# Kernel tuning notes

Measured on AMD Instinct MI355X. Metric: run time of the kernel, lower is better.

## Reference

```python
import jax, jax.numpy as jnp
import numpy as np


def setup_inputs() -> dict:
    key = jax.random.key(0)
    k1, k2, k3, k4 = jax.random.split(key, 4)
    B, Cin, H, W = 16, 64, 96, 96
    D, O, KH, KW, S = 100, 256, 3, 3, 3
    x = jax.random.normal(k1, (B, Cin, H, W), dtype=jnp.float32)
    dictionary = jax.random.normal(k2, (D, Cin, KH, KW), dtype=jnp.float32) * 0.05
    lookup_coefficients = jax.random.normal(k3, (O, KH, KW, S), dtype=jnp.float32) * 0.1
    lookup_indices = jax.random.randint(k4, (O, KH, KW, S), 0, D, dtype=jnp.int64)
    return {
        "x": x,
        "dictionary": dictionary,
        "lookup_coefficients": lookup_coefficients,
        "lookup_indices": lookup_indices,
    }


def reference(x, dictionary, lookup_coefficients, lookup_indices):
    # Dense conv with the small dictionary: [B, Cin, H, W] x [D, Cin, kh, kw] -> [B, D, Oh, Ow]
    conv_out = jax.lax.conv_general_dilated(
        x, dictionary,
        window_strides=(1, 1),
        padding=((1, 1), (1, 1)),
        dimension_numbers=("NCHW", "OIHW", "NCHW"),
    )
    O = lookup_coefficients.shape[0]
    D = dictionary.shape[0]
    # Flatten kernel-position and sparsity axes: each (position, slot) contributes
    # coeff * conv_out[:, idx] to output channel o; COO duplicates sum.
    idx = lookup_indices.reshape(O, -1)      # [O, P*S]
    coeff = lookup_coefficients.reshape(O, -1)  # [O, P*S]
    # Scatter-add into a per-output-channel weight over dictionary entries: W[o, d]
    Wmat = jnp.zeros((O, D), dtype=conv_out.dtype).at[jnp.arange(O)[:, None], idx].add(coeff)
    # Gather-weighted-sum == sparse (O x D) matmul against conv_out channels
    out = jnp.einsum("od,bdhw->bohw", Wmat, conv_out)
    return out
```

## Files before the change

### kernel.cpp

```cpp
#include <hip/hip_runtime.h>

#define NB   16
#define CIN  64
#define HH   96
#define WW   96
#define DD   100
#define OO   256
#define NWG  (NB * HH)

typedef __attribute__((ext_vector_type(8))) short  bf16x8;
typedef __attribute__((ext_vector_type(4))) float  f32x4;

#define FSWZ(wp) ((((wp) ^ ((wp) >> 3)) & 7) << 4)

static __device__ __forceinline__ unsigned short f32_to_bf16(float f) {
    unsigned int u = __float_as_uint(f);
    u += 0x7FFFu + ((u >> 16) & 1u);
    return (unsigned short)(u >> 16);
}

__global__ __launch_bounds__(256) void prep_kernel(
    const float* __restrict__ x, const float* __restrict__ dict,
    const float* __restrict__ coeff, const int* __restrict__ idx,
    unsigned short* __restrict__ x2, unsigned short* __restrict__ weff2,
    unsigned short* __restrict__ zbuf)
{
    __shared__ unsigned short lds[CIN * 100];
    __shared__ float wrow[DD];
    const int blk = blockIdx.x, tid = threadIdx.x;

    if (blk < NWG) {
        const int b = blk / HH, h = blk % HH;
        for (int it = 0; it < 6; ++it) {
            int i = tid + it * 256;
            int c = i / 24, w4 = i % 24;
            float4 v = *reinterpret_cast<const float4*>(
                x + (((size_t)(b * CIN + c) * HH + h) * WW + w4 * 4));
            ushort4 u;
            u.x = f32_to_bf16(v.x); u.y = f32_to_bf16(v.y);
            u.z = f32_to_bf16(v.z); u.w = f32_to_bf16(v.w);
            *reinterpret_cast<ushort4*>(&lds[c * 100 + w4 * 4]) = u;
        }
        __syncthreads();
        for (int it = 0; it < 6; ++it) {
            int i = tid + it * 256;
            int w = i / 16, c = (i % 16) * 4;
            ushort4 u;
            u.x = lds[(c + 0) * 100 + w];
            u.y = lds[(c + 1) * 100 + w];
            u.z = lds[(c + 2) * 100 + w];
            u.w = lds[(c + 3) * 100 + w];
            *reinterpret_cast<ushort4*>(x2 + (((size_t)(b * HH + h) * WW + w) * CIN + c)) = u;
        }
    } else {
        const int o = blk - NWG;
        if (o == 0 && tid < 8) zbuf[tid] = 0;
        if (tid < DD) wrow[tid] = 0.f;
        __syncthreads();
        if (tid == 0) {
            for (int s = 0; s < 27; ++s) wrow[idx[o * 27 + s]] += coeff[o * 27 + s];
        }
        __syncthreads();
        for (int j = tid; j < 576; j += 256) {
            int kpos = j >> 6, c = j & 63;
            float s = 0.f;
            for (int d = 0; d < DD; ++d)
                s += wrow[d] * dict[d * 576 + c * 9 + kpos];
            int otile = o >> 4, ks = c >> 5;
            int lane8 = (o & 15) | (((c >> 3) & 3) << 4);
            weff2[((size_t)(kpos * 32 + otile * 2 + ks)) * 512 + lane8 * 8 + (c & 7)]
                = f32_to_bf16(s);
        }
    }
}

__global__ __launch_bounds__(512, 4) void conv_kernel(
    const unsigned short* __restrict__ x2,
    const unsigned short* __restrict__ weff2,
    const unsigned short* __restrict__ zbuf,
    float* __restrict__ out)
{
    __shared__ unsigned short xs[3 * 98 * 64];

    const int wg  = blockIdx.x;
    const int swz = (wg & 7) * (NWG / 8) + (wg >> 3);
    const int b = swz / HH, h = swz % HH;
    const int tid = threadIdx.x;
    const int lane = tid & 63, wid = tid >> 6;
    const int wm = wid >> 2, wn = wid & 3;

    char* xsb = reinterpret_cast<char*>(xs);

    const unsigned short* wbase = weff2 + (size_t)(wn * 8) * 512 + lane * 8;
    bf16x8 bfr[4][4];
#pragma unroll
    for (int s = 0; s < 4; ++s)
#pragma unroll
        for (int n = 0; n < 4; ++n)
            bfr[s][n] = *reinterpret_cast<const bf16x8*>(
                wbase + (((s >> 1) * 32) + n * 2 + (s & 1)) * 512);

    const char* x2b = reinterpret_cast<const char*>(x2) + (size_t)b * HH * WW * 128;
#pragma unroll
    for (int it = 0; it < 5; ++it) {
        int chunk = tid + it * 512;
        if (chunk < 2352) {
            int r = chunk / 784, rem = chunk % 784;
            int wp = rem >> 3, gb = (rem & 7) << 4;
            int hp = h - 1 + r;
            const char* src;
            if (wp >= 1 && wp <= 96 && hp >= 0 && hp < HH)
                src = x2b + ((size_t)(hp * WW + wp - 1) * 128 + (gb ^ FSWZ(wp)));
            else
                src = reinterpret_cast<const char*>(zbuf);
            __builtin_amdgcn_global_load_lds(
                (const __attribute__((address_space(1))) void*)src,
                (__attribute__((address_space(3))) void*)(xsb + chunk * 16),
                16, 0, 0);
        }
    }

    f32x4 acc[3][4];
#pragma unroll
    for (int m = 0; m < 3; ++m)
#pragma unroll
        for (int n = 0; n < 4; ++n)
            acc[m][n] = (f32x4){0.f, 0.f, 0.f, 0.f};

    __syncthreads();

    const int wb16 = wm * 48 + (lane & 15);

#pragma unroll
    for (int s = 0; s < 18; ++s) {
        const int kpos = s >> 1, ks = s & 1;
        const int kh = kpos / 3, dw = kpos % 3;
        const int cb = (ks * 32 + (lane >> 4) * 8) * 2;
        bf16x8 a[3];
#pragma unroll
        for (int m = 0; m < 3; ++m) {
            int wpos = wb16 + m * 16 + dw;
            a[m] = *reinterpret_cast<const bf16x8*>(
                xsb + kh * 12544 + wpos * 128 + (cb ^ FSWZ(wpos)));
        }
#pragma unroll
        for (int m = 0; m < 3; ++m)
#pragma unroll
            for (int n = 0; n < 4; ++n)
                acc[m][n] = __builtin_amdgcn_mfma_f32_16x16x32_bf16(
                    a[m], bfr[s & 3][n], acc[m][n], 0, 0, 0);
        if (s < 14) {
            const int s4 = s + 4;
            const int off = (s4 >> 1) * 32 + (s4 & 1);
#pragma unroll
            for (int n = 0; n < 4; ++n)
                bfr[s & 3][n] = *reinterpret_cast<const bf16x8*>(
                    wbase + (off + n * 2) * 512);
        }
    }

#pragma unroll
    for (int m = 0; m < 3; ++m)
#pragma unroll
        for (int n = 0; n < 4; ++n) {
            int o = wn * 64 + n * 16 + (lane & 15);
            int w = wm * 48 + m * 16 + (lane >> 4) * 4;
            *reinterpret_cast<f32x4*>(
                out + (((size_t)(b * OO + o) * HH + h) * WW + w)) = acc[m][n];
        }
}

extern "C" void kernel_launch(void* const* d_in, const int* in_sizes, int n_in,
                              void* d_out, int out_size, void* d_ws, size_t ws_size,
                              hipStream_t stream) {
    const float* x     = (const float*)d_in[0];
    const float* dict  = (const float*)d_in[1];
    const float* coeff = (const float*)d_in[2];
    const int*   idx   = (const int*)d_in[3];
    float* out = (float*)d_out;

    char* ws = (char*)d_ws;
    unsigned short* weff2 = (unsigned short*)ws;
    unsigned short* zbuf  = (unsigned short*)(ws + 294912);
    unsigned short* x2    = (unsigned short*)(ws + 1048576);

    prep_kernel<<<NWG + OO, 256, 0, stream>>>(x, dict, coeff, idx, x2, weff2, zbuf);
    conv_kernel<<<NWG, 512, 0, stream>>>(x2, weff2, zbuf, out);
}
```

Baseline: 82.16 us.

## Split each conv row into two half-width workgroups with 8 output-channel waves

Each workgroup now covers half an output row (48 columns) instead of the full row, which doubles the grid. Its 8 waves split the 256 output channels 32 apiece, where before they formed a 2x4 width-by-channel grid. This halves the LDS tile and the per-wave accumulator and B-fragment registers, which should allow more occupancy and better latency hiding. The cost is a larger halo overlap in the loaded input, more global reads of the weights overall, and a shallower weight-prefetch pipeline (two steps ahead instead of four).

Result: no change. 80.74 us (-1.7%).

```diff
diff --git a/kernel.cpp b/kernel.cpp
--- a/kernel.cpp
+++ b/kernel.cpp
@@ -7,6 +7,8 @@
 #define DD   100
 #define OO   256
 #define NWG  (NB * HH)
+#define NCV  (NB * HH * 2)
+#define WPAD 50
 
 typedef __attribute__((ext_vector_type(8))) short  bf16x8;
 typedef __attribute__((ext_vector_type(4))) float  f32x4;
@@ -80,39 +82,38 @@
     const unsigned short* __restrict__ zbuf,
     float* __restrict__ out)
 {
-    __shared__ unsigned short xs[3 * 98 * 64];
+    __shared__ unsigned short xs[3 * WPAD * 64];
 
     const int wg  = blockIdx.x;
-    const int swz = (wg & 7) * (NWG / 8) + (wg >> 3);
-    const int b = swz / HH, h = swz % HH;
+    const int swz = (wg & 7) * (NCV / 8) + (wg >> 3);
+    const int b = swz / 192, rem = swz % 192;
+    const int h = rem >> 1, ws = (rem & 1) * 48;
     const int tid = threadIdx.x;
     const int lane = tid & 63, wid = tid >> 6;
-    const int wm = wid >> 2, wn = wid & 3;
 
     char* xsb = reinterpret_cast<char*>(xs);
+    const char* x2b = reinterpret_cast<const char*>(x2) + (size_t)b * HH * WW * 128;
+    const char* zbp = reinterpret_cast<const char*>(zbuf);
 
-    const unsigned short* wbase = weff2 + (size_t)(wn * 8) * 512 + lane * 8;
-    bf16x8 bfr[4][4];
+    const unsigned short* wbase = weff2 + (size_t)(wid * 4) * 512 + lane * 8;
+    bf16x8 bA[2], bB[2];
 #pragma unroll
-    for (int s = 0; s < 4; ++s)
+    for (int n = 0; n < 2; ++n)
+        bA[n] = *reinterpret_cast<const bf16x8*>(wbase + (n * 2 + 0) * 512);
 #pragma unroll
-        for (int n = 0; n < 4; ++n)
-            bfr[s][n] = *reinterpret_cast<const bf16x8*>(
-                wbase + (((s >> 1) * 32) + n * 2 + (s & 1)) * 512);
+    for (int n = 0; n < 2; ++n)
+        bB[n] = *reinterpret_cast<const bf16x8*>(wbase + (n * 2 + 1) * 512);
 
-    const char* x2b = reinterpret_cast<const char*>(x2) + (size_t)b * HH * WW * 128;
 #pragma unroll
-    for (int it = 0; it < 5; ++it) {
+    for (int it = 0; it < 3; ++it) {
         int chunk = tid + it * 512;
-        if (chunk < 2352) {
-            int r = chunk / 784, rem = chunk % 784;
-            int wp = rem >> 3, gb = (rem & 7) << 4;
-            int hp = h - 1 + r;
-            const char* src;
-            if (wp >= 1 && wp <= 96 && hp >= 0 && hp < HH)
-                src = x2b + ((size_t)(hp * WW + wp - 1) * 128 + (gb ^ FSWZ(wp)));
-            else
-                src = reinterpret_cast<const char*>(zbuf);
+        if (chunk < 1200) {
+            int r = chunk / 400, rem2 = chunk % 400;
+            int wp = rem2 >> 3, gb = (rem2 & 7) << 4;
+            int hp = h - 1 + r, w = ws - 1 + wp;
+            const char* src = (w >= 0 && w < WW && hp >= 0 && hp < HH)
+                ? x2b + ((size_t)(hp * WW + w) * 128 + (gb ^ FSWZ(wp)))
+                : zbp;
             __builtin_amdgcn_global_load_lds(
                 (const __attribute__((address_space(1))) void*)src,
                 (__attribute__((address_space(3))) void*)(xsb + chunk * 16),
@@ -120,16 +121,16 @@
         }
     }
 
-    f32x4 acc[3][4];
+    f32x4 acc[3][2];
 #pragma unroll
     for (int m = 0; m < 3; ++m)
 #pragma unroll
-        for (int n = 0; n < 4; ++n)
+        for (int n = 0; n < 2; ++n)
             acc[m][n] = (f32x4){0.f, 0.f, 0.f, 0.f};
 
     __syncthreads();
 
-    const int wb16 = wm * 48 + (lane & 15);
+    const int l15 = lane & 15;
 
 #pragma unroll
     for (int s = 0; s < 18; ++s) {
@@ -139,32 +140,33 @@
         bf16x8 a[3];
 #pragma unroll
         for (int m = 0; m < 3; ++m) {
-            int wpos = wb16 + m * 16 + dw;
+            int wpos = m * 16 + l15 + dw;
             a[m] = *reinterpret_cast<const bf16x8*>(
-                xsb + kh * 12544 + wpos * 128 + (cb ^ FSWZ(wpos)));
+                xsb + kh * 6400 + wpos * 128 + (cb ^ FSWZ(wpos)));
         }
 #pragma unroll
         for (int m = 0; m < 3; ++m)
 #pragma unroll
-            for (int n = 0; n < 4; ++n)
+            for (int n = 0; n < 2; ++n)
                 acc[m][n] = __builtin_amdgcn_mfma_f32_16x16x32_bf16(
-                    a[m], bfr[s & 3][n], acc[m][n], 0, 0, 0);
-        if (s < 14) {
-            const int s4 = s + 4;
-            const int off = (s4 >> 1) * 32 + (s4 & 1);
+                    a[m], (s & 1) ? bB[n] : bA[n], acc[m][n], 0, 0, 0);
+        if (s < 16) {
+            const int s2 = s + 2;
+            const int off = (s2 >> 1) * 32 + (s2 & 1);
 #pragma unroll
-            for (int n = 0; n < 4; ++n)
-                bfr[s & 3][n] = *reinterpret_cast<const bf16x8*>(
-                    wbase + (off + n * 2) * 512);
+            for (int n = 0; n < 2; ++n) {
+                bf16x8 v = *reinterpret_cast<const bf16x8*>(wbase + (off + n * 2) * 512);
+                if ((s & 1) == 0) bA[n] = v; else bB[n] = v;
+            }
         }
     }
 
 #pragma unroll
     for (int m = 0; m < 3; ++m)
 #pragma unroll
-        for (int n = 0; n < 4; ++n) {
-            int o = wn * 64 + n * 16 + (lane & 15);
-            int w = wm * 48 + m * 16 + (lane >> 4) * 4;
+        for (int n = 0; n < 2; ++n) {
+            int o = wid * 32 + n * 16 + l15;
+            int w = ws + m * 16 + (lane >> 4) * 4;
             *reinterpret_cast<f32x4*>(
                 out + (((size_t)(b * OO + o) * HH + h) * WW + w)) = acc[m][n];
         }
@@ -185,5 +187,5 @@
     unsigned short* x2    = (unsigned short*)(ws + 1048576);
 
     prep_kernel<<<NWG + OO, 256, 0, stream>>>(x, dict, coeff, idx, x2, weff2, zbuf);
-    conv_kernel<<<NWG, 512, 0, stream>>>(x2, weff2, zbuf, out);
+    conv_kernel<<<NCV, 512, 0, stream>>>(x2, weff2, zbuf, out);
 }
```
